# Performance work log

Hardware: AMD Instinct MI355X
Metric: run time of the kernel (lower is better)

## Reference

```python
import jax, jax.numpy as jnp
import numpy as np

B = 16
N_IN_PER = 256
N_SKIP_PER = 1024
C_IN = 256
C_SKIP = 128


def setup_inputs() -> dict:
    key = jax.random.key(0)
    ks = jax.random.split(key, 8)
    n_in = B * N_IN_PER
    n_skip = B * N_SKIP_PER
    in_x = jax.random.normal(ks[0], (n_in, C_IN), dtype=jnp.float32)
    in_pos = jax.random.uniform(ks[1], (n_in, 3), dtype=jnp.float32)
    in_batch = jnp.repeat(jnp.arange(B, dtype=jnp.int64), N_IN_PER)
    skip_x = jax.random.normal(ks[2], (n_skip, C_SKIP), dtype=jnp.float32)
    skip_pos = jax.random.uniform(ks[3], (n_skip, 3), dtype=jnp.float32)
    skip_batch = jnp.repeat(jnp.arange(B, dtype=jnp.int64), N_SKIP_PER)
    d_cat = C_IN + C_SKIP + 3  # 387
    W1 = jax.random.normal(ks[4], (d_cat, 256), dtype=jnp.float32) * (1.0 / np.sqrt(d_cat))
    b1 = jnp.zeros((256,), dtype=jnp.float32)
    W2 = jax.random.normal(ks[5], (256, 256), dtype=jnp.float32) * (1.0 / 16.0)
    b2 = jnp.zeros((256,), dtype=jnp.float32)
    return {"in_x": in_x, "in_pos": in_pos, "in_batch": in_batch,
            "skip_x": skip_x, "skip_pos": skip_pos, "skip_batch": skip_batch,
            "W1": W1, "b1": b1, "W2": W2, "b2": b2, "knn_num": 3}


def _knn_interpolate(in_x, in_pos, in_batch, skip_pos, skip_batch, k):
    # Pairwise squared distances fine->coarse, masked across graphs. [Ns, Ni]
    d2 = jnp.sum((skip_pos[:, None, :] - in_pos[None, :, :]) ** 2, axis=-1)
    cross = skip_batch[:, None] != in_batch[None, :]
    d2 = jnp.where(cross, jnp.inf, d2)
    _, idx = jax.lax.top_k(-d2, k)  # [Ns, k] nearest coarse neighbors
    nb_pos = in_pos[idx]  # [Ns, k, 3]
    dist = jnp.sqrt(jnp.sum((nb_pos - skip_pos[:, None, :]) ** 2, axis=-1))
    dist = jnp.maximum(dist, 1e-10)
    w = 1.0 / dist
    w = w / (jnp.sum(w, axis=-1, keepdims=True) + 1e-16)  # per-target normalization
    return jnp.einsum('nk,nkc->nc', w, in_x[idx])  # [Ns, C_in]


def reference(in_x, in_pos, in_batch, skip_x, skip_pos, skip_batch, W1, b1, W2, b2, knn_num):
    interp = _knn_interpolate(in_x, in_pos, in_batch, skip_pos, skip_batch, knn_num)
    h = jnp.concatenate([interp, skip_x, skip_pos], axis=1)  # [Ns, 387]
    h = jax.nn.relu(h @ W1 + b1)
    h = jax.nn.relu(h @ W2 + b2)
    return h
```

## Files before the change

kernel.cpp:

```cpp
#include <hip/hip_runtime.h>
#include <hip/hip_bf16.h>


typedef __bf16 bf16x8 __attribute__((ext_vector_type(8)));
typedef float  f32x4  __attribute__((ext_vector_type(4)));

__device__ __forceinline__ unsigned short f2bf(float f) {
  __hip_bfloat16 h = __float2bfloat16(f);
  return __builtin_bit_cast(unsigned short, h);
}

#define GLDS16(G, L)                                                          \
  __builtin_amdgcn_global_load_lds(                                           \
      (const __attribute__((address_space(1))) void*)(G),                     \
      (__attribute__((address_space(3))) void*)(L), 16, 0, 0)

static constexpr int MROWS  = 16384;
static constexpr int KPAD   = 416;
static constexpr int KREAL  = 387;

__global__ __launch_bounds__(256) void prep_weights(
    const float* __restrict__ W1, const float* __restrict__ W2,
    unsigned short* __restrict__ W1t, unsigned short* __restrict__ W2t)
{
  const int k = blockIdx.x;
  const int n = threadIdx.x;
  {
    float v = (k < KREAL) ? W1[(size_t)k * 256 + n] : 0.f;
    W1t[(size_t)n * KPAD + k] = f2bf(v);
  }
  if (k < 256) {
    W2t[(size_t)n * 256 + k] = f2bf(W2[(size_t)k * 256 + n]);
  }
}

__global__ __launch_bounds__(256) void knn_build_h(
    const float* __restrict__ in_x,
    const float* __restrict__ in_pos,
    const float* __restrict__ skip_x,
    const float* __restrict__ skip_pos,
    unsigned short* __restrict__ H)
{
  __shared__ float P[3][256];
  const int tid = threadIdx.x;
  const int s0  = blockIdx.x << 2;
  const int ib  = (s0 >> 10) << 8;
  {
    const float* bp = in_pos + (size_t)ib * 3;
    for (int i = tid; i < 768; i += 256) P[i % 3][i / 3] = bp[i];
  }
  __syncthreads();

  const int wid = tid >> 6, lane = tid & 63;
  const int s = s0 + wid;
  const float sx = skip_pos[(size_t)s * 3 + 0];
  const float sy = skip_pos[(size_t)s * 3 + 1];
  const float sz = skip_pos[(size_t)s * 3 + 2];

  float d2[4];
#pragma unroll
  for (int q = 0; q < 4; ++q) {
    const int i = lane + (q << 6);
    const float dx = __fsub_rn(sx, P[0][i]);
    const float dy = __fsub_rn(sy, P[1][i]);
    const float dz = __fsub_rn(sz, P[2][i]);
    d2[q] = __fadd_rn(__fadd_rn(__fmul_rn(dx, dx), __fmul_rn(dy, dy)),
                      __fmul_rn(dz, dz));
  }

  int   gsel[3];
  float wsel[3];
  float wsum = 0.f;
#pragma unroll
  for (int p = 0; p < 3; ++p) {
    float bd = d2[0];
    int   bi = lane;
#pragma unroll
    for (int q = 1; q < 4; ++q) {
      const int i = lane + (q << 6);
      if (d2[q] < bd) { bd = d2[q]; bi = i; }
    }
#pragma unroll
    for (int m = 1; m < 64; m <<= 1) {
      const float od = __shfl_xor(bd, m);
      const int   oi = __shfl_xor(bi, m);
      if (od < bd || (od == bd && oi < bi)) { bd = od; bi = oi; }
    }
    if ((bi & 63) == lane) d2[bi >> 6] = 3.4e38f;
    gsel[p] = bi;
    const float dx = __fsub_rn(P[0][bi], sx);
    const float dy = __fsub_rn(P[1][bi], sy);
    const float dz = __fsub_rn(P[2][bi], sz);
    float dist = sqrtf(__fadd_rn(__fadd_rn(__fmul_rn(dx, dx), __fmul_rn(dy, dy)),
                                 __fmul_rn(dz, dz)));
    dist = fmaxf(dist, 1e-10f);
    const float w = 1.0f / dist;
    wsel[p] = w;
    wsum += w;
  }
  const float denom = wsum + 1e-16f;
  const float w0 = wsel[0] / denom;
  const float w1 = wsel[1] / denom;
  const float w2 = wsel[2] / denom;

  const f32x4* x0 = (const f32x4*)(in_x + (size_t)(ib + gsel[0]) * 256);
  const f32x4* x1 = (const f32x4*)(in_x + (size_t)(ib + gsel[1]) * 256);
  const f32x4* x2 = (const f32x4*)(in_x + (size_t)(ib + gsel[2]) * 256);
  const f32x4 a = x0[lane], b = x1[lane], c = x2[lane];

  unsigned short* hr = H + (size_t)s * KPAD;
  ushort4 o4;
  o4.x = f2bf(w0 * a.x + w1 * b.x + w2 * c.x);
  o4.y = f2bf(w0 * a.y + w1 * b.y + w2 * c.y);
  o4.z = f2bf(w0 * a.z + w1 * b.z + w2 * c.z);
  o4.w = f2bf(w0 * a.w + w1 * b.w + w2 * c.w);
  *(ushort4*)(hr + (lane << 2)) = o4;

  const float2 sv = ((const float2*)(skip_x + (size_t)s * 128))[lane];
  ushort2 o2;
  o2.x = f2bf(sv.x);
  o2.y = f2bf(sv.y);
  *(ushort2*)(hr + 256 + (lane << 1)) = o2;

  if (lane < 32) {
    float v = (lane == 0) ? sx : (lane == 1) ? sy : (lane == 2) ? sz : 0.f;
    hr[384 + lane] = f2bf(v);
  }
}

template <int K, bool OUT_BF16>
__global__ __launch_bounds__(256) void gemm_bt_relu(
    const unsigned short* __restrict__ A,
    const unsigned short* __restrict__ Bt,
    const float* __restrict__ bias,
    void* __restrict__ Out)
{
  __shared__ unsigned short As[128 * 32];
  __shared__ unsigned short Bs[128 * 32];
  const int tid = threadIdx.x, lane = tid & 63, wid = tid >> 6;
  const int m0 = blockIdx.x << 7, n0 = blockIdx.y << 7;

  const int srow = tid >> 2;
  const int scol = (tid & 3) << 3;
  const unsigned short* gA0 = A + (size_t)(m0 + srow) * K + scol;
  const unsigned short* gA1 = gA0 + (size_t)64 * K;
  const unsigned short* gB0 = Bt + (size_t)(n0 + srow) * K + scol;
  const unsigned short* gB1 = gB0 + (size_t)64 * K;
  unsigned short* lA0 = As + wid * 512;
  unsigned short* lA1 = As + 2048 + wid * 512;
  unsigned short* lB0 = Bs + wid * 512;
  unsigned short* lB1 = Bs + 2048 + wid * 512;

  const int wr = (wid >> 1) << 6;
  const int wc = (wid & 1) << 6;
  const int fr = lane & 15;
  const int ko = (lane >> 4) << 3;

  f32x4 acc[4][4] = {};

  for (int ks = 0; ks < K / 32; ++ks) {
    const int k0 = ks << 5;
    GLDS16(gA0 + k0, lA0);
    GLDS16(gA1 + k0, lA1);
    GLDS16(gB0 + k0, lB0);
    GLDS16(gB1 + k0, lB1);
    __syncthreads();
    bf16x8 af[4], bf[4];
#pragma unroll
    for (int m = 0; m < 4; ++m)
      af[m] = *(const bf16x8*)&As[(wr + m * 16 + fr) * 32 + ko];
#pragma unroll
    for (int n = 0; n < 4; ++n)
      bf[n] = *(const bf16x8*)&Bs[(wc + n * 16 + fr) * 32 + ko];
#pragma unroll
    for (int m = 0; m < 4; ++m)
#pragma unroll
      for (int n = 0; n < 4; ++n)
        acc[m][n] =
            __builtin_amdgcn_mfma_f32_16x16x32_bf16(af[m], bf[n], acc[m][n], 0, 0, 0);
    __syncthreads();
  }

  const int r0 = m0 + wr + ((lane >> 4) << 2);
  const int c0 = n0 + wc + fr;
  float bn[4];
#pragma unroll
  for (int n = 0; n < 4; ++n) bn[n] = bias[c0 + n * 16];
#pragma unroll
  for (int m = 0; m < 4; ++m) {
#pragma unroll
    for (int j = 0; j < 4; ++j) {
      const size_t row = (size_t)(r0 + m * 16 + j);
#pragma unroll
      for (int n = 0; n < 4; ++n) {
        const float v = fmaxf(acc[m][n][j] + bn[n], 0.f);
        if constexpr (OUT_BF16)
          ((unsigned short*)Out)[row * 256 + c0 + n * 16] = f2bf(v);
        else
          ((float*)Out)[row * 256 + c0 + n * 16] = v;
      }
    }
  }
}

extern "C" void kernel_launch(void* const* d_in, const int* in_sizes, int n_in,
                              void* d_out, int out_size, void* d_ws, size_t ws_size,
                              hipStream_t stream) {
  const float* in_x     = (const float*)d_in[0];
  const float* in_pos   = (const float*)d_in[1];
  const float* skip_x   = (const float*)d_in[3];
  const float* skip_pos = (const float*)d_in[4];
  const float* W1       = (const float*)d_in[6];
  const float* bias1    = (const float*)d_in[7];
  const float* W2       = (const float*)d_in[8];
  const float* bias2    = (const float*)d_in[9];

  char* ws = (char*)d_ws;
  unsigned short* H   = (unsigned short*)(ws);
  unsigned short* h1  = (unsigned short*)(ws + 13631488);
  unsigned short* W1t = (unsigned short*)(ws + 13631488 + 8388608);
  unsigned short* W2t = (unsigned short*)(ws + 13631488 + 8388608 + 212992);

  prep_weights<<<dim3(KPAD), dim3(256), 0, stream>>>(W1, W2, W1t, W2t);
  knn_build_h<<<dim3(MROWS / 4), dim3(256), 0, stream>>>(in_x, in_pos, skip_x,
                                                         skip_pos, H);
  gemm_bt_relu<KPAD, true><<<dim3(MROWS / 128, 2), dim3(256), 0, stream>>>(
      H, W1t, bias1, (void*)h1);
  gemm_bt_relu<256, false><<<dim3(MROWS / 128, 2), dim3(256), 0, stream>>>(
      h1, W2t, bias2, d_out);
}
```

Measured before the change: 48.58 us.

## Fuse kNN interpolation and both MLP GEMMs into one kernel

Replaces the kNN-build kernel and the two GEMM launches with a single kernel. Each 64-row block builds its concatenated input tile in LDS, runs layer 1 against double-buffered swizzled weight tiles, keeps the hidden activations in LDS, runs layer 2 and writes fp32 output. The weight prep now uses an LDS-tiled transpose with vectorized stores. This removes the HBM round trips for H and h1 and two launches, at the cost of serial per-wave kNN work inside the GEMM block, heavy LDS use that may lower occupancy, and a grid of only 256 blocks.

```diff
diff --git a/kernel.cpp b/kernel.cpp
--- a/kernel.cpp
+++ b/kernel.cpp
@@ -15,192 +15,264 @@
       (const __attribute__((address_space(1))) void*)(G),                     \
       (__attribute__((address_space(3))) void*)(L), 16, 0, 0)
 
-static constexpr int MROWS  = 16384;
-static constexpr int KPAD   = 416;
-static constexpr int KREAL  = 387;
-
-__global__ __launch_bounds__(256) void prep_weights(
+#define BAR()    __builtin_amdgcn_s_barrier()
+#define WAITV(N) asm volatile("s_waitcnt vmcnt(" #N ")" ::: "memory")
+#define WAITL()  asm volatile("s_waitcnt lgkmcnt(0)" ::: "memory")
+
+static constexpr int MROWS = 16384;
+static constexpr int KPAD  = 416;
+static constexpr int KREAL = 387;
+static constexpr int NK1   = 13;
+static constexpr int NK2   = 8;
+static constexpr int HSTR  = 424;
+static constexpr int H1STR = 264;
+
+__global__ __launch_bounds__(256) void prep_w(
     const float* __restrict__ W1, const float* __restrict__ W2,
     unsigned short* __restrict__ W1t, unsigned short* __restrict__ W2t)
 {
-  const int k = blockIdx.x;
-  const int n = threadIdx.x;
-  {
-    float v = (k < KREAL) ? W1[(size_t)k * 256 + n] : 0.f;
-    W1t[(size_t)n * KPAD + k] = f2bf(v);
-  }
-  if (k < 256) {
-    W2t[(size_t)n * 256 + k] = f2bf(W2[(size_t)k * 256 + n]);
-  }
-}
-
-__global__ __launch_bounds__(256) void knn_build_h(
+  __shared__ float T[64][65];
+  int b = blockIdx.x;
+  const float* S; unsigned short* D; int KP, Kreal, kb, nb;
+  if (b < 28) { S = W1; D = W1t; KP = KPAD; Kreal = KREAL; kb = b >> 2; nb = b & 3; }
+  else { b -= 28; S = W2; D = W2t; KP = 256; Kreal = 256; kb = b >> 2; nb = b & 3; }
+  const int k0 = kb << 6, n0 = nb << 6;
+  const int tr = threadIdx.x >> 4, tc = threadIdx.x & 15;
+#pragma unroll
+  for (int i = 0; i < 4; ++i) {
+    const int k = k0 + i * 16 + tr;
+    float4 v = make_float4(0.f, 0.f, 0.f, 0.f);
+    if (k < Kreal) v = *(const float4*)(S + (size_t)k * 256 + n0 + tc * 4);
+    T[i * 16 + tr][tc * 4 + 0] = v.x;
+    T[i * 16 + tr][tc * 4 + 1] = v.y;
+    T[i * 16 + tr][tc * 4 + 2] = v.z;
+    T[i * 16 + tr][tc * 4 + 3] = v.w;
+  }
+  __syncthreads();
+#pragma unroll
+  for (int i = 0; i < 4; ++i) {
+    const int n = n0 + i * 16 + tr;
+    const int k = k0 + tc * 4;
+    if (k < KP) {
+      ushort4 o;
+      o.x = f2bf(T[tc * 4 + 0][i * 16 + tr]);
+      o.y = f2bf(T[tc * 4 + 1][i * 16 + tr]);
+      o.z = f2bf(T[tc * 4 + 2][i * 16 + tr]);
+      o.w = f2bf(T[tc * 4 + 3][i * 16 + tr]);
+      *(ushort4*)(D + (size_t)n * KP + k) = o;
+    }
+  }
+}
+
+__device__ __forceinline__ void stage_tile(const unsigned short* __restrict__ W,
+                                           int Krow, int ks,
+                                           unsigned short* buf, int tid, int wid)
+{
+#pragma unroll
+  for (int ro = 0; ro < 4; ++ro) {
+    const int r  = ro * 64 + (tid >> 2);
+    const int c  = tid & 3;
+    const int cs = c ^ ((r >> 1) & 3);
+    const unsigned short* src = W + (size_t)r * Krow + ks * 32 + cs * 8;
+    unsigned short* dst = buf + ro * 2048 + wid * 512;
+    GLDS16(src, dst);
+  }
+}
+
+__global__ __launch_bounds__(256) void fp_fused(
     const float* __restrict__ in_x,
     const float* __restrict__ in_pos,
     const float* __restrict__ skip_x,
     const float* __restrict__ skip_pos,
-    unsigned short* __restrict__ H)
+    const unsigned short* __restrict__ W1t,
+    const unsigned short* __restrict__ W2t,
+    const float* __restrict__ bias1, const float* __restrict__ bias2,
+    float* __restrict__ out)
 {
-  __shared__ float P[3][256];
-  const int tid = threadIdx.x;
-  const int s0  = blockIdx.x << 2;
-  const int ib  = (s0 >> 10) << 8;
+  __shared__ unsigned short Hs[64 * HSTR];
+  __shared__ unsigned short Bst[2 * 8192];
+  __shared__ float Ps[768];
+
+  const int tid  = threadIdx.x, lane = tid & 63, wid = tid >> 6;
+  const int m0   = blockIdx.x << 6;
+  const int ib   = (m0 >> 10) << 8;
+  const int fr   = lane & 15, g = lane >> 4;
+  const int wc   = wid << 6;
+
+  f32x4 b1v[4], b2v[4];
+#pragma unroll
+  for (int mc = 0; mc < 4; ++mc) {
+    b1v[mc] = *(const f32x4*)(bias1 + wc + mc * 16 + g * 4);
+    b2v[mc] = *(const f32x4*)(bias2 + wc + mc * 16 + g * 4);
+  }
+
   {
     const float* bp = in_pos + (size_t)ib * 3;
-    for (int i = tid; i < 768; i += 256) P[i % 3][i / 3] = bp[i];
-  }
-  __syncthreads();
-
-  const int wid = tid >> 6, lane = tid & 63;
-  const int s = s0 + wid;
-  const float sx = skip_pos[(size_t)s * 3 + 0];
-  const float sy = skip_pos[(size_t)s * 3 + 1];
-  const float sz = skip_pos[(size_t)s * 3 + 2];
-
-  float d2[4];
+#pragma unroll
+    for (int i = tid; i < 768; i += 256) Ps[(i % 3) * 256 + i / 3] = bp[i];
+  }
+  WAITL(); BAR();
+
+  stage_tile(W1t, KPAD, 0, Bst, tid, wid);
+  stage_tile(W1t, KPAD, 1, Bst + 8192, tid, wid);
+
+  float Pxr[4], Pyr[4], Pzr[4];
 #pragma unroll
   for (int q = 0; q < 4; ++q) {
-    const int i = lane + (q << 6);
-    const float dx = __fsub_rn(sx, P[0][i]);
-    const float dy = __fsub_rn(sy, P[1][i]);
-    const float dz = __fsub_rn(sz, P[2][i]);
-    d2[q] = __fadd_rn(__fadd_rn(__fmul_rn(dx, dx), __fmul_rn(dy, dy)),
-                      __fmul_rn(dz, dz));
-  }
-
-  int   gsel[3];
-  float wsel[3];
-  float wsum = 0.f;
-#pragma unroll
-  for (int p = 0; p < 3; ++p) {
-    float bd = d2[0];
-    int   bi = lane;
-#pragma unroll
-    for (int q = 1; q < 4; ++q) {
-      const int i = lane + (q << 6);
-      if (d2[q] < bd) { bd = d2[q]; bi = i; }
-    }
-#pragma unroll
-    for (int m = 1; m < 64; m <<= 1) {
-      const float od = __shfl_xor(bd, m);
-      const int   oi = __shfl_xor(bi, m);
-      if (od < bd || (od == bd && oi < bi)) { bd = od; bi = oi; }
-    }
-    if ((bi & 63) == lane) d2[bi >> 6] = 3.4e38f;
-    gsel[p] = bi;
-    const float dx = __fsub_rn(P[0][bi], sx);
-    const float dy = __fsub_rn(P[1][bi], sy);
-    const float dz = __fsub_rn(P[2][bi], sz);
-    float dist = sqrtf(__fadd_rn(__fadd_rn(__fmul_rn(dx, dx), __fmul_rn(dy, dy)),
-                                 __fmul_rn(dz, dz)));
-    dist = fmaxf(dist, 1e-10f);
-    const float w = 1.0f / dist;
-    wsel[p] = w;
-    wsum += w;
-  }
-  const float denom = wsum + 1e-16f;
-  const float w0 = wsel[0] / denom;
-  const float w1 = wsel[1] / denom;
-  const float w2 = wsel[2] / denom;
-
-  const f32x4* x0 = (const f32x4*)(in_x + (size_t)(ib + gsel[0]) * 256);
-  const f32x4* x1 = (const f32x4*)(in_x + (size_t)(ib + gsel[1]) * 256);
-  const f32x4* x2 = (const f32x4*)(in_x + (size_t)(ib + gsel[2]) * 256);
-  const f32x4 a = x0[lane], b = x1[lane], c = x2[lane];
-
-  unsigned short* hr = H + (size_t)s * KPAD;
-  ushort4 o4;
-  o4.x = f2bf(w0 * a.x + w1 * b.x + w2 * c.x);
-  o4.y = f2bf(w0 * a.y + w1 * b.y + w2 * c.y);
-  o4.z = f2bf(w0 * a.z + w1 * b.z + w2 * c.z);
-  o4.w = f2bf(w0 * a.w + w1 * b.w + w2 * c.w);
-  *(ushort4*)(hr + (lane << 2)) = o4;
-
-  const float2 sv = ((const float2*)(skip_x + (size_t)s * 128))[lane];
-  ushort2 o2;
-  o2.x = f2bf(sv.x);
-  o2.y = f2bf(sv.y);
-  *(ushort2*)(hr + 256 + (lane << 1)) = o2;
-
-  if (lane < 32) {
-    float v = (lane == 0) ? sx : (lane == 1) ? sy : (lane == 2) ? sz : 0.f;
-    hr[384 + lane] = f2bf(v);
-  }
-}
-
-template <int K, bool OUT_BF16>
-__global__ __launch_bounds__(256) void gemm_bt_relu(
-    const unsigned short* __restrict__ A,
-    const unsigned short* __restrict__ Bt,
-    const float* __restrict__ bias,
-    void* __restrict__ Out)
-{
-  __shared__ unsigned short As[128 * 32];
-  __shared__ unsigned short Bs[128 * 32];
-  const int tid = threadIdx.x, lane = tid & 63, wid = tid >> 6;
-  const int m0 = blockIdx.x << 7, n0 = blockIdx.y << 7;
-
-  const int srow = tid >> 2;
-  const int scol = (tid & 3) << 3;
-  const unsigned short* gA0 = A + (size_t)(m0 + srow) * K + scol;
-  const unsigned short* gA1 = gA0 + (size_t)64 * K;
-  const unsigned short* gB0 = Bt + (size_t)(n0 + srow) * K + scol;
-  const unsigned short* gB1 = gB0 + (size_t)64 * K;
-  unsigned short* lA0 = As + wid * 512;
-  unsigned short* lA1 = As + 2048 + wid * 512;
-  unsigned short* lB0 = Bs + wid * 512;
-  unsigned short* lB1 = Bs + 2048 + wid * 512;
-
-  const int wr = (wid >> 1) << 6;
-  const int wc = (wid & 1) << 6;
-  const int fr = lane & 15;
-  const int ko = (lane >> 4) << 3;
+    Pxr[q] = Ps[lane + q * 64];
+    Pyr[q] = Ps[256 + lane + q * 64];
+    Pzr[q] = Ps[512 + lane + q * 64];
+  }
+  float spv = 0.f;
+  if (lane < 48) spv = skip_pos[(size_t)(m0 + wid * 16) * 3 + lane];
+
+  for (int p = 0; p < 16; ++p) {
+    const int lr = wid * 16 + p;
+    const int s  = m0 + lr;
+    const float sx = __shfl(spv, 3 * p + 0);
+    const float sy = __shfl(spv, 3 * p + 1);
+    const float sz = __shfl(spv, 3 * p + 2);
+
+    float d2[4];
+#pragma unroll
+    for (int q = 0; q < 4; ++q) {
+      const float dx = __fsub_rn(sx, Pxr[q]);
+      const float dy = __fsub_rn(sy, Pyr[q]);
+      const float dz = __fsub_rn(sz, Pzr[q]);
+      d2[q] = __fadd_rn(__fadd_rn(__fmul_rn(dx, dx), __fmul_rn(dy, dy)),
+                        __fmul_rn(dz, dz));
+    }
+    int gsel[3]; float wsel[3]; float wsum = 0.f;
+#pragma unroll
+    for (int t = 0; t < 3; ++t) {
+      float bd = d2[0]; int bi = lane;
+#pragma unroll
+      for (int q = 1; q < 4; ++q) {
+        const int i = lane + (q << 6);
+        if (d2[q] < bd) { bd = d2[q]; bi = i; }
+      }
+#pragma unroll
+      for (int mk = 1; mk < 64; mk <<= 1) {
+        const float od = __shfl_xor(bd, mk);
+        const int   oi = __shfl_xor(bi, mk);
+        if (od < bd || (od == bd && oi < bi)) { bd = od; bi = oi; }
+      }
+      const bool win = ((bi & 63) == lane);
+      const int  qw  = bi >> 6;
+      d2[0] = (win && qw == 0) ? 3.4e38f : d2[0];
+      d2[1] = (win && qw == 1) ? 3.4e38f : d2[1];
+      d2[2] = (win && qw == 2) ? 3.4e38f : d2[2];
+      d2[3] = (win && qw == 3) ? 3.4e38f : d2[3];
+      gsel[t] = bi;
+      const float w = 1.0f / fmaxf(sqrtf(bd), 1e-10f);
+      wsel[t] = w; wsum += w;
+    }
+    const float denom = wsum + 1e-16f;
+    const float w0 = wsel[0] / denom, w1 = wsel[1] / denom, w2 = wsel[2] / denom;
+
+    const f32x4 a = *(const f32x4*)(in_x + (size_t)(ib + gsel[0]) * 256 + lane * 4);
+    const f32x4 b = *(const f32x4*)(in_x + (size_t)(ib + gsel[1]) * 256 + lane * 4);
+    const f32x4 c = *(const f32x4*)(in_x + (size_t)(ib + gsel[2]) * 256 + lane * 4);
+    ushort4 o4;
+    o4.x = f2bf(w0 * a.x + w1 * b.x + w2 * c.x);
+    o4.y = f2bf(w0 * a.y + w1 * b.y + w2 * c.y);
+    o4.z = f2bf(w0 * a.z + w1 * b.z + w2 * c.z);
+    o4.w = f2bf(w0 * a.w + w1 * b.w + w2 * c.w);
+    *(ushort4*)&Hs[lr * HSTR + lane * 4] = o4;
+
+    const float2 sv = *(const float2*)(skip_x + (size_t)s * 128 + lane * 2);
+    ushort2 o2; o2.x = f2bf(sv.x); o2.y = f2bf(sv.y);
+    *(ushort2*)&Hs[lr * HSTR + 256 + lane * 2] = o2;
+
+    if (lane < 40) {
+      const float v = (lane == 0) ? sx : (lane == 1) ? sy : (lane == 2) ? sz : 0.f;
+      Hs[lr * HSTR + 384 + lane] = f2bf(v);
+    }
+  }
+  WAITL(); BAR();
+
+  int woff[4], h1off[4], h2off[4];
+#pragma unroll
+  for (int i = 0; i < 4; ++i) {
+    const int R = wc + i * 16 + fr;
+    woff[i]  = R * 32 + ((g ^ ((R >> 1) & 3)) << 3);
+    h1off[i] = (i * 16 + fr) * HSTR + g * 8;
+    h2off[i] = (i * 16 + fr) * H1STR + g * 8;
+  }
 
   f32x4 acc[4][4] = {};
 
-  for (int ks = 0; ks < K / 32; ++ks) {
-    const int k0 = ks << 5;
-    GLDS16(gA0 + k0, lA0);
-    GLDS16(gA1 + k0, lA1);
-    GLDS16(gB0 + k0, lB0);
-    GLDS16(gB1 + k0, lB1);
-    __syncthreads();
-    bf16x8 af[4], bf[4];
-#pragma unroll
-    for (int m = 0; m < 4; ++m)
-      af[m] = *(const bf16x8*)&As[(wr + m * 16 + fr) * 32 + ko];
-#pragma unroll
-    for (int n = 0; n < 4; ++n)
-      bf[n] = *(const bf16x8*)&Bs[(wc + n * 16 + fr) * 32 + ko];
-#pragma unroll
-    for (int m = 0; m < 4; ++m)
-#pragma unroll
-      for (int n = 0; n < 4; ++n)
-        acc[m][n] =
-            __builtin_amdgcn_mfma_f32_16x16x32_bf16(af[m], bf[n], acc[m][n], 0, 0, 0);
-    __syncthreads();
-  }
-
-  const int r0 = m0 + wr + ((lane >> 4) << 2);
-  const int c0 = n0 + wc + fr;
-  float bn[4];
-#pragma unroll
-  for (int n = 0; n < 4; ++n) bn[n] = bias[c0 + n * 16];
-#pragma unroll
-  for (int m = 0; m < 4; ++m) {
-#pragma unroll
-    for (int j = 0; j < 4; ++j) {
-      const size_t row = (size_t)(r0 + m * 16 + j);
-#pragma unroll
-      for (int n = 0; n < 4; ++n) {
-        const float v = fmaxf(acc[m][n][j] + bn[n], 0.f);
-        if constexpr (OUT_BF16)
-          ((unsigned short*)Out)[row * 256 + c0 + n * 16] = f2bf(v);
-        else
-          ((float*)Out)[row * 256 + c0 + n * 16] = v;
-      }
-    }
-  }
+#pragma unroll 1
+  for (int ks = 0; ks < NK1; ++ks) {
+    if (ks < NK1 - 1) { WAITV(4); } else { WAITV(0); }
+    BAR();
+    const unsigned short* bb = Bst + (ks & 1) * 8192;
+    bf16x8 wf[4], hf[4];
+#pragma unroll
+    for (int i = 0; i < 4; ++i) wf[i] = *(const bf16x8*)&bb[woff[i]];
+#pragma unroll
+    for (int i = 0; i < 4; ++i) hf[i] = *(const bf16x8*)&Hs[h1off[i] + ks * 32];
+#pragma unroll
+    for (int mc = 0; mc < 4; ++mc)
+#pragma unroll
+      for (int rr = 0; rr < 4; ++rr)
+        acc[mc][rr] = __builtin_amdgcn_mfma_f32_16x16x32_bf16(
+            wf[mc], hf[rr], acc[mc][rr], 0, 0, 0);
+    WAITL(); BAR();
+    if (ks + 2 < NK1) stage_tile(W1t, KPAD, ks + 2, Bst + (ks & 1) * 8192, tid, wid);
+  }
+
+  stage_tile(W2t, 256, 0, Bst, tid, wid);
+  stage_tile(W2t, 256, 1, Bst + 8192, tid, wid);
+
+  unsigned short* h1s = Hs;
+#pragma unroll
+  for (int rr = 0; rr < 4; ++rr)
+#pragma unroll
+    for (int mc = 0; mc < 4; ++mc) {
+      ushort4 o;
+      o.x = f2bf(fmaxf(acc[mc][rr][0] + b1v[mc][0], 0.f));
+      o.y = f2bf(fmaxf(acc[mc][rr][1] + b1v[mc][1], 0.f));
+      o.z = f2bf(fmaxf(acc[mc][rr][2] + b1v[mc][2], 0.f));
+      o.w = f2bf(fmaxf(acc[mc][rr][3] + b1v[mc][3], 0.f));
+      *(ushort4*)&h1s[(rr * 16 + fr) * H1STR + wc + mc * 16 + g * 4] = o;
+    }
+  WAITL(); BAR();
+
+#pragma unroll
+  for (int mc = 0; mc < 4; ++mc)
+#pragma unroll
+    for (int rr = 0; rr < 4; ++rr) acc[mc][rr] = f32x4{0.f, 0.f, 0.f, 0.f};
+
+#pragma unroll 1
+  for (int ks = 0; ks < NK2; ++ks) {
+    if (ks < NK2 - 1) { WAITV(4); } else { WAITV(0); }
+    BAR();
+    const unsigned short* bb = Bst + (ks & 1) * 8192;
+    bf16x8 wf[4], hf[4];
+#pragma unroll
+    for (int i = 0; i < 4; ++i) wf[i] = *(const bf16x8*)&bb[woff[i]];
+#pragma unroll
+    for (int i = 0; i < 4; ++i) hf[i] = *(const bf16x8*)&h1s[h2off[i] + ks * 32];
+#pragma unroll
+    for (int mc = 0; mc < 4; ++mc)
+#pragma unroll
+      for (int rr = 0; rr < 4; ++rr)
+        acc[mc][rr] = __builtin_amdgcn_mfma_f32_16x16x32_bf16(
+            wf[mc], hf[rr], acc[mc][rr], 0, 0, 0);
+    WAITL(); BAR();
+    if (ks + 2 < NK2) stage_tile(W2t, 256, ks + 2, Bst + (ks & 1) * 8192, tid, wid);
+  }
+
+#pragma unroll
+  for (int rr = 0; rr < 4; ++rr)
+#pragma unroll
+    for (int mc = 0; mc < 4; ++mc) {
+      f32x4 o;
+#pragma unroll
+      for (int j = 0; j < 4; ++j) o[j] = fmaxf(acc[mc][rr][j] + b2v[mc][j], 0.f);
+      *(f32x4*)(out + (size_t)(m0 + rr * 16 + fr) * 256 + wc + mc * 16 + g * 4) = o;
+    }
 }
 
 extern "C" void kernel_launch(void* const* d_in, const int* in_sizes, int n_in,
@@ -216,16 +288,10 @@
   const float* bias2    = (const float*)d_in[9];
 
   char* ws = (char*)d_ws;
-  unsigned short* H   = (unsigned short*)(ws);
-  unsigned short* h1  = (unsigned short*)(ws + 13631488);
-  unsigned short* W1t = (unsigned short*)(ws + 13631488 + 8388608);
-  unsigned short* W2t = (unsigned short*)(ws + 13631488 + 8388608 + 212992);
-
-  prep_weights<<<dim3(KPAD), dim3(256), 0, stream>>>(W1, W2, W1t, W2t);
-  knn_build_h<<<dim3(MROWS / 4), dim3(256), 0, stream>>>(in_x, in_pos, skip_x,
-                                                         skip_pos, H);
-  gemm_bt_relu<KPAD, true><<<dim3(MROWS / 128, 2), dim3(256), 0, stream>>>(
-      H, W1t, bias1, (void*)h1);
-  gemm_bt_relu<256, false><<<dim3(MROWS / 128, 2), dim3(256), 0, stream>>>(
-      h1, W2t, bias2, d_out);
-}
+  unsigned short* W1t = (unsigned short*)(ws);
+  unsigned short* W2t = (unsigned short*)(ws + 212992);
+
+  prep_w<<<dim3(44), dim3(256), 0, stream>>>(W1, W2, W1t, W2t);
+  fp_fused<<<dim3(MROWS / 64), dim3(256), 0, stream>>>(
+      in_x, in_pos, skip_x, skip_pos, W1t, W2t, bias1, bias2, (float*)d_out);
+}
```

Measured after the change: 67.56 us. +39.1%, slower.
